# Optimization experiments

Hardware: AMD Instinct MI355X
Metric: run time of the kernel (lower is better)

The kernel has to match this reference:

```python
import jax, jax.numpy as jnp
import numpy as np

H = 2048       # hidden_size
F = 1024       # moe_intermediate_size
E = 32         # n_routed_experts
G = 8          # n_group
TOPK_GROUP = 3
TOP_K = 6      # num_experts_per_tok
N_SHARED = 2
SCALE = 1.0    # routed_scaling_factor
B, S = 1, 2048


def setup_inputs() -> dict:
    key = jax.random.key(0)
    ks = jax.random.split(key, 8)
    std = 0.02
    return {
        "hidden_states": jax.random.normal(ks[0], (B, S, H), dtype=jnp.float32),
        "w_gate": jax.random.normal(ks[1], (E, H), dtype=jnp.float32) * std,
        "wg": jax.random.normal(ks[2], (E, H, F), dtype=jnp.float32) * std,  # stacked gate_proj
        "wu": jax.random.normal(ks[3], (E, H, F), dtype=jnp.float32) * std,  # stacked up_proj
        "wd": jax.random.normal(ks[4], (E, F, H), dtype=jnp.float32) * std,  # stacked down_proj
        "sg": jax.random.normal(ks[5], (N_SHARED * F, H), dtype=jnp.float32) * std,  # shared gate_proj
        "su": jax.random.normal(ks[6], (N_SHARED * F, H), dtype=jnp.float32) * std,  # shared up_proj
        "sd": jax.random.normal(ks[7], (H, N_SHARED * F), dtype=jnp.float32) * std,  # shared down_proj
    }


def reference(hidden_states, w_gate, wg, wu, wd, sg, su, sd):
    b, s, h = hidden_states.shape
    x = hidden_states.reshape(-1, h)                    # [T, H]
    T = x.shape[0]

    # ---- MoEGate (softmax scoring, group_limited_greedy top-k) ----
    logits = x.astype(jnp.float32) @ w_gate.T           # [T, E]
    scores = jax.nn.softmax(logits, axis=-1)
    group_scores = scores.reshape(T, G, E // G).max(axis=-1)          # [T, G]
    _, group_idx = jax.lax.top_k(group_scores, TOPK_GROUP)            # [T, topk_group]
    group_mask = jax.nn.one_hot(group_idx, G, dtype=scores.dtype).sum(axis=1)  # [T, G]
    score_mask = jnp.repeat(group_mask, E // G, axis=-1)              # [T, E]
    tmp_scores = jnp.where(score_mask > 0.5, scores, 0.0)
    topk_weight, topk_idx = jax.lax.top_k(tmp_scores, TOP_K)          # [T, K]
    # norm_topk_prob=True, top_k>1
    topk_weight = topk_weight / (topk_weight.sum(axis=-1, keepdims=True) + 1e-20) * SCALE

    # combine weights per (token, expert): scatter topk weights (indices distinct)
    combine_w = jnp.zeros((T, E), dtype=jnp.float32)
    combine_w = combine_w.at[jnp.arange(T)[:, None], topk_idx].add(topk_weight)

    # ---- routed experts: dense grouped GEMMs, weighted combine ----
    g = jnp.einsum('th,ehf->etf', x, wg)                # [E, T, F]
    u = jnp.einsum('th,ehf->etf', x, wu)                # [E, T, F]
    act = jax.nn.silu(g) * u                            # SiLU gated
    act = act * combine_w.T[:, :, None]                 # fold combine weights before down-proj
    y = jnp.einsum('etf,efh->th', act, wd)              # [T, H]

    # ---- shared experts ----
    shared = (jax.nn.silu(x @ sg.T) * (x @ su.T)) @ sd.T

    return (y + shared).reshape(b, s, h)
```

## Files before the change

kernel.cpp:

```cpp
#include <hip/hip_runtime.h>

#define HD   2048
#define FD   1024
#define NEXP 32
#define TOPK 6
#define TT   2048
#define SDIM 2048
#define NPAIR (TT*TOPK)

typedef __bf16 bf16x8 __attribute__((ext_vector_type(8)));
typedef float  f32x4  __attribute__((ext_vector_type(4)));

#define GLOAD_LDS16(g, l) __builtin_amdgcn_global_load_lds( \
    (const __attribute__((address_space(1))) void*)(g),     \
    (__attribute__((address_space(3))) void*)(l), 16, 0, 0)

#define WAIT_VM3  asm volatile("s_waitcnt vmcnt(3)" ::: "memory")
#define WAIT_VM0  asm volatile("s_waitcnt vmcnt(0)" ::: "memory")
#define BAR() do { __builtin_amdgcn_s_barrier(); } while (0)

__device__ __forceinline__ ushort f2b(float f) {
  __bf16 h = (__bf16)f;
  union { __bf16 h; ushort u; } v; v.h = h;
  return v.u;
}
__device__ __forceinline__ float b2f(ushort u) {
  union { unsigned u; float f; } v; v.u = (unsigned)u << 16;
  return v.f;
}

__device__ __forceinline__ int xcd_swz(int bid, int nact) {
  int xcd = bid & 7, i = bid >> 3;
  int q = nact >> 3, r = nact & 7;
  int base = (xcd < r) ? xcd * (q + 1) : r * (q + 1) + (xcd - r) * q;
  return base + i;
}

__device__ __forceinline__ void argmax32(float &v, int &i) {
  #pragma unroll
  for (int m = 16; m >= 1; m >>= 1) {
    float ov = __shfl_xor(v, m, 32);
    int   oi = __shfl_xor(i, m, 32);
    if (ov > v || (ov == v && oi < i)) { v = ov; i = oi; }
  }
}

__global__ __launch_bounds__(64) void gating_kernel(
    const float* __restrict__ x, const float* __restrict__ wgate,
    int* __restrict__ topk_idx, float* __restrict__ topk_w, int* __restrict__ cnt)
{
  int t = blockIdx.x;
  int l = threadIdx.x;
  int e = l & 31;
  int half = l >> 5;
  const float* xr = x + (size_t)t * HD + half * (HD/2);
  const float* wr = wgate + (size_t)e * HD + half * (HD/2);
  float acc = 0.f;
  for (int i = 0; i < HD/2; i += 4) {
    float4 a = *(const float4*)(xr + i);
    float4 b = *(const float4*)(wr + i);
    acc += a.x*b.x + a.y*b.y + a.z*b.z + a.w*b.w;
  }
  acc += __shfl_xor(acc, 32);
  float logit = acc;
  float mx = logit;
  #pragma unroll
  for (int m = 16; m >= 1; m >>= 1) mx = fmaxf(mx, __shfl_xor(mx, m, 32));
  float p = __expf(logit - mx);
  float s = p;
  #pragma unroll
  for (int m = 16; m >= 1; m >>= 1) s += __shfl_xor(s, m, 32);
  float score = p / s;
  float gs = score;
  gs = fmaxf(gs, __shfl_xor(gs, 1, 32));
  gs = fmaxf(gs, __shfl_xor(gs, 2, 32));
  int g = e >> 2;
  float gw = gs;
  bool ingroup = false;
  for (int r = 0; r < 3; ++r) {
    float v = gw; int gi = g;
    argmax32(v, gi);
    if (g == gi) { ingroup = true; gw = -1.f; }
  }
  float ms = ingroup ? score : 0.f;
  int myrank = -1;
  float denom = 1e-20f;
  float mw = ms;
  for (int r = 0; r < 6; ++r) {
    float v = mw; int ei = e;
    argmax32(v, ei);
    denom += v;
    if (e == ei) { myrank = r; mw = -1.f; }
  }
  if (l < 32 && myrank >= 0) {
    topk_idx[t*TOPK + myrank] = e;
    topk_w  [t*TOPK + myrank] = score / denom;
    atomicAdd(&cnt[e], 1);
  }
}

__global__ void scan_kernel(const int* __restrict__ cnt, int* __restrict__ offs,
                            int* __restrict__ tl_e, int* __restrict__ tl_m, int* __restrict__ ntl) {
  if (threadIdx.x == 0) {
    int o = 0, nt = 0;
    for (int e = 0; e < NEXP; ++e) {
      offs[e] = o;
      for (int m = 0; m < cnt[e]; m += 256) { tl_e[nt] = e; tl_m[nt] = m; ++nt; }
      o += cnt[e];
    }
    ntl[0] = nt;
  }
}

__global__ void fill_kernel(const int* __restrict__ topk_idx, const float* __restrict__ topk_w,
                            const int* __restrict__ offs, int* __restrict__ cur,
                            int* __restrict__ pair_tok, float* __restrict__ pair_w,
                            int* __restrict__ inv)
{
  int idx = blockIdx.x * blockDim.x + threadIdx.x;
  if (idx >= NPAIR) return;
  int e = topk_idx[idx];
  int p = offs[e] + atomicAdd(&cur[e], 1);
  pair_tok[p] = idx / TOPK;
  pair_w[p]   = topk_w[idx];
  inv[idx]    = p;
}

__global__ __launch_bounds__(256) void fconv4(
    const float* __restrict__ s0, const float* __restrict__ s1,
    const float* __restrict__ s2, const float* __restrict__ s3,
    ushort* __restrict__ d0, ushort* __restrict__ d1,
    ushort* __restrict__ d2, ushort* __restrict__ d3)
{
  int sel = blockIdx.y;
  const float* in = (sel == 0) ? s0 : (sel == 1) ? s1 : (sel == 2) ? s2 : s3;
  ushort* out = (sel == 0) ? d0 : (sel == 1) ? d1 : (sel == 2) ? d2 : d3;
  int i = blockIdx.x * blockDim.x + threadIdx.x;
  float4 v = ((const float4*)in)[i];
  ((ushort4*)out)[i] = make_ushort4(f2b(v.x), f2b(v.y), f2b(v.z), f2b(v.w));
}

#define TSTR 76
__global__ __launch_bounds__(256) void tconv2(
    const float* __restrict__ in0, const float* __restrict__ in1,
    ushort* __restrict__ out0, ushort* __restrict__ out1, int R, int C)
{
  __shared__ ushort T[64*TSTR];
  const float* inz = blockIdx.z ? in1 : in0;
  ushort* outz = blockIdx.z ? out1 : out0;
  int tiles_c = C >> 6;
  int bt = blockIdx.x;
  int r0 = (bt / tiles_c) << 6;
  int c0 = (bt % tiles_c) << 6;
  const float* src = inz + (size_t)blockIdx.y * R * C;
  ushort* dst = outz + (size_t)blockIdx.y * R * C;
  int t = threadIdx.x;
  int row = (t >> 4) << 2;
  int col4 = (t & 15) << 2;
  float vv[4][4];
  #pragma unroll
  for (int i = 0; i < 4; ++i) {
    float4 v = *(const float4*)(src + (size_t)(r0 + row + i) * C + c0 + col4);
    vv[i][0] = v.x; vv[i][1] = v.y; vv[i][2] = v.z; vv[i][3] = v.w;
  }
  #pragma unroll
  for (int cc = 0; cc < 4; ++cc)
    *(ushort4*)&T[(col4 + cc)*TSTR + row] =
      make_ushort4(f2b(vv[0][cc]), f2b(vv[1][cc]), f2b(vv[2][cc]), f2b(vv[3][cc]));
  __syncthreads();
  #pragma unroll
  for (int p = 0; p < 2; ++p) {
    int item = t + p*256;
    int oc = item >> 3, seg = item & 7;
    ushort4 a = *(const ushort4*)&T[oc*TSTR + seg*8];
    ushort4 b = *(const ushort4*)&T[oc*TSTR + seg*8 + 4];
    ushort* d = dst + (size_t)(c0 + oc) * R + r0 + seg*8;
    *(ushort4*)(d)     = a;
    *(ushort4*)(d + 4) = b;
  }
}

__global__ __launch_bounds__(256) void combine_kernel(
    const ushort* __restrict__ pairout, const int* __restrict__ inv, float* __restrict__ y)
{
  int t = blockIdx.x;
  int h0 = threadIdx.x * 8;
  const int* iv = inv + t*TOPK;
  float* yr = y + (size_t)t * HD + h0;
  float4 y0 = *(const float4*)(yr);
  float4 y1 = *(const float4*)(yr + 4);
  float acc[8] = {y0.x, y0.y, y0.z, y0.w, y1.x, y1.y, y1.z, y1.w};
  #pragma unroll
  for (int r = 0; r < TOPK; ++r) {
    int p = iv[r];
    const ushort* pr = pairout + (size_t)p * HD + h0;
    ushort4 a = *(const ushort4*)(pr);
    ushort4 b = *(const ushort4*)(pr + 4);
    acc[0] += b2f(a.x); acc[1] += b2f(a.y); acc[2] += b2f(a.z); acc[3] += b2f(a.w);
    acc[4] += b2f(b.x); acc[5] += b2f(b.y); acc[6] += b2f(b.z); acc[7] += b2f(b.w);
  }
  *(float4*)(yr)     = make_float4(acc[0], acc[1], acc[2], acc[3]);
  *(float4*)(yr + 4) = make_float4(acc[4], acc[5], acc[6], acc[7]);
}


__global__ __launch_bounds__(512, 4) void gu_routed_b(
    const ushort* __restrict__ xb, const ushort* __restrict__ wgt, const ushort* __restrict__ wut,
    const int* __restrict__ pair_tok, const float* __restrict__ pair_w,
    const int* __restrict__ cnt, const int* __restrict__ offs,
    const int* __restrict__ tl_e, const int* __restrict__ tl_m, const int* __restrict__ ntl,
    ushort* __restrict__ act)
{
  __shared__ ushort A[3][256*32];
  __shared__ ushort Bg[3][64*32];
  __shared__ ushort Bu[3][64*32];

  int nact = ntl[0] * 16;
  int bid = blockIdx.x;
  if (bid >= nact) return;
  int wid = xcd_swz(bid, nact);
  int tile = wid >> 4;
  int nt = wid & 15;
  int e  = tl_e[tile];
  int m0 = tl_m[tile];
  int ce = cnt[e];
  int oe = offs[e];
  int n0 = nt * 64;
  int tid = threadIdx.x, lane = tid & 63, w = tid >> 6;

  int csrc = (lane & 3) ^ ((lane >> 3) & 3);
  const ushort* asrc[2];
  #pragma unroll
  for (int j = 0; j < 2; ++j) {
    int r = (2*w + j)*16 + (lane >> 2);
    int pi = min(m0 + r, ce - 1);
    asrc[j] = xb + (size_t)pair_tok[oe + pi] * HD + csrc * 8;
  }
  int tsel = w >> 2;
  int bw = w & 3;
  const ushort* bsrc = (tsel ? wut : wgt) +
      ((size_t)e * FD + n0 + bw*16 + (lane >> 2)) * HD + csrc * 8;
  ushort* bdst0 = tsel ? &Bu[0][bw*512] : &Bg[0][bw*512];
  ushort* bdst1 = tsel ? &Bu[1][bw*512] : &Bg[1][bw*512];
  ushort* bdst2 = tsel ? &Bu[2][bw*512] : &Bg[2][bw*512];

  int lm = lane & 15, lg = lane >> 4;
  int wr = w >> 1, wc = w & 1;
  int asw = (lm >> 1) & 3;

  f32x4 accg[4][2], accu[4][2];
  #pragma unroll
  for (int m = 0; m < 4; ++m)
    #pragma unroll
    for (int n = 0; n < 2; ++n) { accg[m][n] = f32x4{0,0,0,0}; accu[m][n] = f32x4{0,0,0,0}; }

  #define GUB_ISSUE(T, BUF, BD) do { \
    GLOAD_LDS16(asrc[0] + (T)*32, &A[BUF][(2*w)*512]); \
    GLOAD_LDS16(asrc[1] + (T)*32, &A[BUF][(2*w+1)*512]); \
    GLOAD_LDS16(bsrc + (T)*32, BD); \
  } while (0)
  #define GUB_COMPUTE(BUF) do { \
    bf16x8 a[4], bg[2], bu[2]; \
    _Pragma("unroll") \
    for (int m = 0; m < 4; ++m) \
      a[m] = *(const bf16x8*)&A[BUF][(wr*64 + m*16 + lm)*32 + (lg ^ asw)*8]; \
    _Pragma("unroll") \
    for (int n = 0; n < 2; ++n) { \
      int row = wc*32 + n*16 + lm; \
      bg[n] = *(const bf16x8*)&Bg[BUF][row*32 + (lg ^ asw)*8]; \
      bu[n] = *(const bf16x8*)&Bu[BUF][row*32 + (lg ^ asw)*8]; \
    } \
    __builtin_amdgcn_s_setprio(1); \
    _Pragma("unroll") \
    for (int m = 0; m < 4; ++m) \
      _Pragma("unroll") \
      for (int n = 0; n < 2; ++n) { \
        accg[m][n] = __builtin_amdgcn_mfma_f32_16x16x32_bf16(a[m], bg[n], accg[m][n], 0, 0, 0); \
        accu[m][n] = __builtin_amdgcn_mfma_f32_16x16x32_bf16(a[m], bu[n], accu[m][n], 0, 0, 0); \
      } \
    __builtin_amdgcn_s_setprio(0); \
  } while (0)

  GUB_ISSUE(0, 0, bdst0);
  GUB_ISSUE(1, 1, bdst1);
  WAIT_VM3;
  BAR();

  for (int tt = 0; tt < 20; ++tt) {
    int t = tt * 3;
    GUB_ISSUE(t+2, 2, bdst2); GUB_COMPUTE(0); WAIT_VM3; BAR();
    GUB_ISSUE(t+3, 0, bdst0); GUB_COMPUTE(1); WAIT_VM3; BAR();
    GUB_ISSUE(t+4, 1, bdst1); GUB_COMPUTE(2); WAIT_VM3; BAR();
  }
  GUB_ISSUE(62, 2, bdst2); GUB_COMPUTE(0); WAIT_VM3; BAR();
  GUB_ISSUE(63, 0, bdst0); GUB_COMPUTE(1); WAIT_VM3; BAR();
  GUB_COMPUTE(2); WAIT_VM0; BAR();
  GUB_COMPUTE(0);
  #undef GUB_ISSUE
  #undef GUB_COMPUTE

  #pragma unroll
  for (int m = 0; m < 4; ++m) {
    #pragma unroll
    for (int j = 0; j < 4; ++j) {
      int rl = wr*64 + m*16 + lg*4 + j;
      int pi = m0 + rl;
      if (pi >= ce) continue;
      float pwv = pair_w[oe + pi];
      size_t base = (size_t)(oe + pi) * FD + n0 + wc*32;
      #pragma unroll
      for (int n = 0; n < 2; ++n) {
        float gv = accg[m][n][j];
        float uv = accu[m][n][j];
        float sv = gv / (1.f + __expf(-gv));
        act[base + n*16 + lm] = f2b(sv * uv * pwv);
      }
    }
  }
}

__global__ __launch_bounds__(512, 4) void down_routed_b(
    const ushort* __restrict__ act, const ushort* __restrict__ wdt,
    const int* __restrict__ cnt, const int* __restrict__ offs,
    const int* __restrict__ tl_e, const int* __restrict__ tl_m, const int* __restrict__ ntl,
    ushort* __restrict__ pairout)
{
  __shared__ ushort A[3][256*32];
  __shared__ ushort Bd[3][128*32];

  int nact = ntl[0] * 16;
  int bid = blockIdx.x;
  if (bid >= nact) return;
  int wid = xcd_swz(bid, nact);
  int tile = wid >> 4;
  int nt = wid & 15;
  int e  = tl_e[tile];
  int m0 = tl_m[tile];
  int ce = cnt[e];
  int oe = offs[e];
  int n0 = nt * 128;
  int tid = threadIdx.x, lane = tid & 63, w = tid >> 6;

  int csrc = (lane & 3) ^ ((lane >> 3) & 3);
  const ushort* asrc[2];
  #pragma unroll
  for (int j = 0; j < 2; ++j) {
    int r = (2*w + j)*16 + (lane >> 2);
    int pi = min(m0 + r, ce - 1);
    asrc[j] = act + (size_t)(oe + pi) * FD + csrc * 8;
  }
  const ushort* bsrc = wdt + ((size_t)e * HD + n0 + w*16 + (lane >> 2)) * FD + csrc * 8;

  int lm = lane & 15, lg = lane >> 4;
  int wr = w >> 1, wc = w & 1;
  int asw = (lm >> 1) & 3;

  f32x4 acc[4][4];
  #pragma unroll
  for (int m = 0; m < 4; ++m)
    #pragma unroll
    for (int n = 0; n < 4; ++n) acc[m][n] = f32x4{0,0,0,0};

  #define DNB_ISSUE(T, BUF) do { \
    GLOAD_LDS16(asrc[0] + (T)*32, &A[BUF][(2*w)*512]); \
    GLOAD_LDS16(asrc[1] + (T)*32, &A[BUF][(2*w+1)*512]); \
    GLOAD_LDS16(bsrc + (T)*32, &Bd[BUF][w*512]); \
  } while (0)
  #define DNB_COMPUTE(BUF) do { \
    bf16x8 a[4], b[4]; \
    _Pragma("unroll") \
    for (int m = 0; m < 4; ++m) \
      a[m] = *(const bf16x8*)&A[BUF][(wr*64 + m*16 + lm)*32 + (lg ^ asw)*8]; \
    _Pragma("unroll") \
    for (int n = 0; n < 4; ++n) { \
      int row = wc*64 + n*16 + lm; \
      b[n] = *(const bf16x8*)&Bd[BUF][row*32 + (lg ^ asw)*8]; \
    } \
    __builtin_amdgcn_s_setprio(1); \
    _Pragma("unroll") \
    for (int m = 0; m < 4; ++m) \
      _Pragma("unroll") \
      for (int n = 0; n < 4; ++n) \
        acc[m][n] = __builtin_amdgcn_mfma_f32_16x16x32_bf16(a[m], b[n], acc[m][n], 0, 0, 0); \
    __builtin_amdgcn_s_setprio(0); \
  } while (0)

  DNB_ISSUE(0, 0);
  DNB_ISSUE(1, 1);
  WAIT_VM3;
  BAR();

  for (int tt = 0; tt < 10; ++tt) {
    int t = tt * 3;
    DNB_ISSUE(t+2, 2); DNB_COMPUTE(0); WAIT_VM3; BAR();
    DNB_ISSUE(t+3, 0); DNB_COMPUTE(1); WAIT_VM3; BAR();
    DNB_ISSUE(t+4, 1); DNB_COMPUTE(2); WAIT_VM3; BAR();
  }
  DNB_COMPUTE(0); WAIT_VM0; BAR();
  DNB_COMPUTE(1);
  #undef DNB_ISSUE
  #undef DNB_COMPUTE

  #pragma unroll
  for (int m = 0; m < 4; ++m) {
    #pragma unroll
    for (int j = 0; j < 4; ++j) {
      int rl = wr*64 + m*16 + lg*4 + j;
      int pi = m0 + rl;
      if (pi >= ce) continue;
      size_t base = (size_t)(oe + pi) * HD + n0 + wc*64;
      #pragma unroll
      for (int n = 0; n < 4; ++n)
        pairout[base + n*16 + lm] = f2b(acc[m][n][j]);
    }
  }
}

__global__ __launch_bounds__(512, 4) void shared_gu_b(
    const ushort* __restrict__ xb, const ushort* __restrict__ sgb, const ushort* __restrict__ sub,
    ushort* __restrict__ sact)
{
  __shared__ ushort A[3][256*32];
  __shared__ ushort Bg[3][64*32];
  __shared__ ushort Bu[3][64*32];

  int bid = blockIdx.x;
  int wid = (bid & 7) * 32 + (bid >> 3);
  int mt = wid & 7;
  int nt = wid >> 3;
  int m0 = mt * 256;
  int n0 = nt * 64;
  int tid = threadIdx.x, lane = tid & 63, w = tid >> 6;

  int csrc = (lane & 3) ^ ((lane >> 3) & 3);
  const ushort* asrc[2];
  #pragma unroll
  for (int j = 0; j < 2; ++j) {
    int r = (2*w + j)*16 + (lane >> 2);
    asrc[j] = xb + (size_t)(m0 + r) * HD + csrc * 8;
  }
  int tsel = w >> 2;
  int bw = w & 3;
  const ushort* bsrc = (tsel ? sub : sgb) + (size_t)(n0 + bw*16 + (lane >> 2)) * HD + csrc * 8;
  ushort* bdst0 = tsel ? &Bu[0][bw*512] : &Bg[0][bw*512];
  ushort* bdst1 = tsel ? &Bu[1][bw*512] : &Bg[1][bw*512];
  ushort* bdst2 = tsel ? &Bu[2][bw*512] : &Bg[2][bw*512];

  int lm = lane & 15, lg = lane >> 4;
  int wr = w >> 1, wc = w & 1;
  int asw = (lm >> 1) & 3;

  f32x4 accg[4][2], accu[4][2];
  #pragma unroll
  for (int m = 0; m < 4; ++m)
    #pragma unroll
    for (int n = 0; n < 2; ++n) { accg[m][n] = f32x4{0,0,0,0}; accu[m][n] = f32x4{0,0,0,0}; }

  #define SGB_ISSUE(T, BUF, BD) do { \
    GLOAD_LDS16(asrc[0] + (T)*32, &A[BUF][(2*w)*512]); \
    GLOAD_LDS16(asrc[1] + (T)*32, &A[BUF][(2*w+1)*512]); \
    GLOAD_LDS16(bsrc + (T)*32, BD); \
  } while (0)
  #define SGB_COMPUTE(BUF) do { \
    bf16x8 a[4], bg[2], bu[2]; \
    _Pragma("unroll") \
    for (int m = 0; m < 4; ++m) \
      a[m] = *(const bf16x8*)&A[BUF][(wr*64 + m*16 + lm)*32 + (lg ^ asw)*8]; \
    _Pragma("unroll") \
    for (int n = 0; n < 2; ++n) { \
      int row = wc*32 + n*16 + lm; \
      bg[n] = *(const bf16x8*)&Bg[BUF][row*32 + (lg ^ asw)*8]; \
      bu[n] = *(const bf16x8*)&Bu[BUF][row*32 + (lg ^ asw)*8]; \
    } \
    __builtin_amdgcn_s_setprio(1); \
    _Pragma("unroll") \
    for (int m = 0; m < 4; ++m) \
      _Pragma("unroll") \
      for (int n = 0; n < 2; ++n) { \
        accg[m][n] = __builtin_amdgcn_mfma_f32_16x16x32_bf16(a[m], bg[n], accg[m][n], 0, 0, 0); \
        accu[m][n] = __builtin_amdgcn_mfma_f32_16x16x32_bf16(a[m], bu[n], accu[m][n], 0, 0, 0); \
      } \
    __builtin_amdgcn_s_setprio(0); \
  } while (0)

  SGB_ISSUE(0, 0, bdst0);
  SGB_ISSUE(1, 1, bdst1);
  WAIT_VM3;
  BAR();

  for (int tt = 0; tt < 20; ++tt) {
    int t = tt * 3;
    SGB_ISSUE(t+2, 2, bdst2); SGB_COMPUTE(0); WAIT_VM3; BAR();
    SGB_ISSUE(t+3, 0, bdst0); SGB_COMPUTE(1); WAIT_VM3; BAR();
    SGB_ISSUE(t+4, 1, bdst1); SGB_COMPUTE(2); WAIT_VM3; BAR();
  }
  SGB_ISSUE(62, 2, bdst2); SGB_COMPUTE(0); WAIT_VM3; BAR();
  SGB_ISSUE(63, 0, bdst0); SGB_COMPUTE(1); WAIT_VM3; BAR();
  SGB_COMPUTE(2); WAIT_VM0; BAR();
  SGB_COMPUTE(0);
  #undef SGB_ISSUE
  #undef SGB_COMPUTE

  #pragma unroll
  for (int m = 0; m < 4; ++m) {
    #pragma unroll
    for (int j = 0; j < 4; ++j) {
      int rl = wr*64 + m*16 + lg*4 + j;
      size_t base = (size_t)(m0 + rl) * SDIM + n0 + wc*32;
      #pragma unroll
      for (int n = 0; n < 2; ++n) {
        float gv = accg[m][n][j];
        float uv = accu[m][n][j];
        float sv = gv / (1.f + __expf(-gv));
        sact[base + n*16 + lm] = f2b(sv * uv);
      }
    }
  }
}

__global__ __launch_bounds__(512, 4) void shared_down_b(
    const ushort* __restrict__ sact, const ushort* __restrict__ sdb, float* __restrict__ y)
{
  __shared__ ushort A[3][256*32];
  __shared__ ushort Bd[3][128*32];

  int bid = blockIdx.x;
  int wid = (bid & 7) * 16 + (bid >> 3);
  int mt = wid & 7;
  int nt = wid >> 3;
  int m0 = mt * 256;
  int n0 = nt * 128;
  int tid = threadIdx.x, lane = tid & 63, w = tid >> 6;

  int csrc = (lane & 3) ^ ((lane >> 3) & 3);
  const ushort* asrc[2];
  #pragma unroll
  for (int j = 0; j < 2; ++j) {
    int r = (2*w + j)*16 + (lane >> 2);
    asrc[j] = sact + (size_t)(m0 + r) * SDIM + csrc * 8;
  }
  const ushort* bsrc = sdb + (size_t)(n0 + w*16 + (lane >> 2)) * SDIM + csrc * 8;

  int lm = lane & 15, lg = lane >> 4;
  int wr = w >> 1, wc = w & 1;
  int asw = (lm >> 1) & 3;

  f32x4 acc[4][4];
  #pragma unroll
  for (int m = 0; m < 4; ++m)
    #pragma unroll
    for (int n = 0; n < 4; ++n) acc[m][n] = f32x4{0,0,0,0};

  #define SDB_ISSUE(T, BUF) do { \
    GLOAD_LDS16(asrc[0] + (T)*32, &A[BUF][(2*w)*512]); \
    GLOAD_LDS16(asrc[1] + (T)*32, &A[BUF][(2*w+1)*512]); \
    GLOAD_LDS16(bsrc + (T)*32, &Bd[BUF][w*512]); \
  } while (0)
  #define SDB_COMPUTE(BUF) do { \
    bf16x8 a[4], b[4]; \
    _Pragma("unroll") \
    for (int m = 0; m < 4; ++m) \
      a[m] = *(const bf16x8*)&A[BUF][(wr*64 + m*16 + lm)*32 + (lg ^ asw)*8]; \
    _Pragma("unroll") \
    for (int n = 0; n < 4; ++n) { \
      int row = wc*64 + n*16 + lm; \
      b[n] = *(const bf16x8*)&Bd[BUF][row*32 + (lg ^ asw)*8]; \
    } \
    __builtin_amdgcn_s_setprio(1); \
    _Pragma("unroll") \
    for (int m = 0; m < 4; ++m) \
      _Pragma("unroll") \
      for (int n = 0; n < 4; ++n) \
        acc[m][n] = __builtin_amdgcn_mfma_f32_16x16x32_bf16(a[m], b[n], acc[m][n], 0, 0, 0); \
    __builtin_amdgcn_s_setprio(0); \
  } while (0)

  SDB_ISSUE(0, 0);
  SDB_ISSUE(1, 1);
  WAIT_VM3;
  BAR();

  for (int tt = 0; tt < 20; ++tt) {
    int t = tt * 3;
    SDB_ISSUE(t+2, 2); SDB_COMPUTE(0); WAIT_VM3; BAR();
    SDB_ISSUE(t+3, 0); SDB_COMPUTE(1); WAIT_VM3; BAR();
    SDB_ISSUE(t+4, 1); SDB_COMPUTE(2); WAIT_VM3; BAR();
  }
  SDB_ISSUE(62, 2); SDB_COMPUTE(0); WAIT_VM3; BAR();
  SDB_ISSUE(63, 0); SDB_COMPUTE(1); WAIT_VM3; BAR();
  SDB_COMPUTE(2); WAIT_VM0; BAR();
  SDB_COMPUTE(0);
  #undef SDB_ISSUE
  #undef SDB_COMPUTE

  #pragma unroll
  for (int m = 0; m < 4; ++m) {
    #pragma unroll
    for (int j = 0; j < 4; ++j) {
      int rl = wr*64 + m*16 + lg*4 + j;
      size_t base = (size_t)(m0 + rl) * HD + n0 + wc*64;
      #pragma unroll
      for (int n = 0; n < 4; ++n)
        y[base + n*16 + lm] = acc[m][n][j];
    }
  }
}

extern "C" void kernel_launch(void* const* d_in, const int* in_sizes, int n_in,
                              void* d_out, int out_size, void* d_ws, size_t ws_size,
                              hipStream_t stream) {
  const float* x     = (const float*)d_in[0];
  const float* wgate = (const float*)d_in[1];
  const float* wg    = (const float*)d_in[2];
  const float* wu    = (const float*)d_in[3];
  const float* wd    = (const float*)d_in[4];
  const float* sg    = (const float*)d_in[5];
  const float* su    = (const float*)d_in[6];
  const float* sd    = (const float*)d_in[7];
  float* y = (float*)d_out;
  char* ws = (char*)d_ws;

  ushort* xb   = (ushort*)(ws + 0);
  ushort* act  = (ushort*)(ws + 8388608);
  ushort* sact = (ushort*)(ws + 33554432);
  int*    tidx = (int*)  (ws + 41943040);
  float*  tw   = (float*)(ws + 41992192);
  int*    ptok = (int*)  (ws + 42041344);
  float*  pw   = (float*)(ws + 42090496);
  int*    cnt  = (int*)  (ws + 42139648);
  int*    curc = (int*)  (ws + 42139776);
  int*    offs = (int*)  (ws + 42139904);
  int*    tl_e = (int*)  (ws + 42140160);
  int*    tl_m = (int*)  (ws + 42140672);
  int*    ntl  = (int*)  (ws + 42141184);
  int*    inv  = (int*)  (ws + 42141440);
  ushort* wgt  = (ushort*)(ws + 50331648);
  ushort* wut  = (ushort*)(ws + 184549376);
  ushort* wdt  = (ushort*)(ws + 318767104);
  ushort* sgb  = (ushort*)(ws + 452984832);
  ushort* sub  = (ushort*)(ws + 461373440);
  ushort* sdb  = (ushort*)(ws + 469762048);
  ushort* pairout = wgt;

  hipMemsetAsync(cnt, 0, 512, stream);

  gating_kernel<<<dim3(TT), dim3(64), 0, stream>>>(x, wgate, tidx, tw, cnt);
  scan_kernel<<<dim3(1), dim3(64), 0, stream>>>(cnt, offs, tl_e, tl_m, ntl);
  fill_kernel<<<dim3(48), dim3(256), 0, stream>>>(tidx, tw, offs, curc, ptok, pw, inv);

  fconv4<<<dim3(4096, 4), dim3(256), 0, stream>>>(x, sg, su, sd, xb, sgb, sub, sdb);
  tconv2<<<dim3(512, NEXP, 2), dim3(256), 0, stream>>>(wg, wu, wgt, wut, HD, FD);
  tconv2<<<dim3(512, NEXP, 1), dim3(256), 0, stream>>>(wd, wd, wdt, wdt, FD, HD);

  shared_gu_b<<<dim3(256), dim3(512), 0, stream>>>(xb, sgb, sub, sact);
  shared_down_b<<<dim3(128), dim3(512), 0, stream>>>(sact, sdb, y);
  gu_routed_b<<<dim3(1280), dim3(512), 0, stream>>>(xb, wgt, wut, ptok, pw, cnt, offs,
                                                    tl_e, tl_m, ntl, act);
  down_routed_b<<<dim3(1280), dim3(512), 0, stream>>>(act, wdt, cnt, offs,
                                                      tl_e, tl_m, ntl, pairout);
  combine_kernel<<<dim3(TT), dim3(256), 0, stream>>>(pairout, inv, y);
}
```

Measured before the change: 733.4 us.

## Load GEMM A operands directly into registers, bypassing LDS, and merge weight transposes

In all four GEMM kernels, the A-operand tile (activations) is no longer staged through LDS. Each wave now loads its own A fragments straight from global memory into registers, double-buffered one K-step ahead, while B still goes through the triple-buffered global-to-LDS path. This cuts LDS footprint and LDS read traffic, but each wave pair now loads the same A rows redundantly and the loads are less coalesced per lane. Separately, the two weight-transpose launches are merged into one three-slice launch to save a kernel launch.

```diff
diff --git a/kernel.cpp b/kernel.cpp
--- a/kernel.cpp
+++ b/kernel.cpp
@@ -15,7 +15,8 @@
     (const __attribute__((address_space(1))) void*)(g),     \
     (__attribute__((address_space(3))) void*)(l), 16, 0, 0)
 
-#define WAIT_VM3  asm volatile("s_waitcnt vmcnt(3)" ::: "memory")
+#define WAIT_VM5  asm volatile("s_waitcnt vmcnt(5)" ::: "memory")
+#define WAIT_VM4  asm volatile("s_waitcnt vmcnt(4)" ::: "memory")
 #define WAIT_VM0  asm volatile("s_waitcnt vmcnt(0)" ::: "memory")
 #define BAR() do { __builtin_amdgcn_s_barrier(); } while (0)
 
@@ -141,13 +142,16 @@
 }
 
 #define TSTR 76
-__global__ __launch_bounds__(256) void tconv2(
-    const float* __restrict__ in0, const float* __restrict__ in1,
-    ushort* __restrict__ out0, ushort* __restrict__ out1, int R, int C)
+__global__ __launch_bounds__(256) void tconv3(
+    const float* __restrict__ iwg, const float* __restrict__ iwu, const float* __restrict__ iwd,
+    ushort* __restrict__ owg, ushort* __restrict__ owu, ushort* __restrict__ owd)
 {
   __shared__ ushort T[64*TSTR];
-  const float* inz = blockIdx.z ? in1 : in0;
-  ushort* outz = blockIdx.z ? out1 : out0;
+  int z = blockIdx.z;
+  const float* inz = (z == 0) ? iwg : (z == 1) ? iwu : iwd;
+  ushort* outz = (z == 0) ? owg : (z == 1) ? owu : owd;
+  int R = (z == 2) ? FD : HD;
+  int C = (z == 2) ? HD : FD;
   int tiles_c = C >> 6;
   int bt = blockIdx.x;
   int r0 = (bt / tiles_c) << 6;
@@ -211,7 +215,6 @@
     const int* __restrict__ tl_e, const int* __restrict__ tl_m, const int* __restrict__ ntl,
     ushort* __restrict__ act)
 {
-  __shared__ ushort A[3][256*32];
   __shared__ ushort Bg[3][64*32];
   __shared__ ushort Bu[3][64*32];
 
@@ -228,14 +231,19 @@
   int n0 = nt * 64;
   int tid = threadIdx.x, lane = tid & 63, w = tid >> 6;
 
+  int lm = lane & 15, lg = lane >> 4;
+  int wr = w >> 1, wc = w & 1;
+  int asw = (lm >> 1) & 3;
+
+  const ushort* ap0; const ushort* ap1; const ushort* ap2; const ushort* ap3;
+  {
+    int r0 = wr*64 + lm;
+    ap0 = xb + (size_t)pair_tok[oe + min(m0 + r0,      ce - 1)] * HD + lg*8;
+    ap1 = xb + (size_t)pair_tok[oe + min(m0 + r0 + 16, ce - 1)] * HD + lg*8;
+    ap2 = xb + (size_t)pair_tok[oe + min(m0 + r0 + 32, ce - 1)] * HD + lg*8;
+    ap3 = xb + (size_t)pair_tok[oe + min(m0 + r0 + 48, ce - 1)] * HD + lg*8;
+  }
   int csrc = (lane & 3) ^ ((lane >> 3) & 3);
-  const ushort* asrc[2];
-  #pragma unroll
-  for (int j = 0; j < 2; ++j) {
-    int r = (2*w + j)*16 + (lane >> 2);
-    int pi = min(m0 + r, ce - 1);
-    asrc[j] = xb + (size_t)pair_tok[oe + pi] * HD + csrc * 8;
-  }
   int tsel = w >> 2;
   int bw = w & 3;
   const ushort* bsrc = (tsel ? wut : wgt) +
@@ -244,26 +252,22 @@
   ushort* bdst1 = tsel ? &Bu[1][bw*512] : &Bg[1][bw*512];
   ushort* bdst2 = tsel ? &Bu[2][bw*512] : &Bg[2][bw*512];
 
-  int lm = lane & 15, lg = lane >> 4;
-  int wr = w >> 1, wc = w & 1;
-  int asw = (lm >> 1) & 3;
-
+  bf16x8 aE0, aE1, aE2, aE3, aO0, aO1, aO2, aO3;
   f32x4 accg[4][2], accu[4][2];
   #pragma unroll
   for (int m = 0; m < 4; ++m)
     #pragma unroll
     for (int n = 0; n < 2; ++n) { accg[m][n] = f32x4{0,0,0,0}; accu[m][n] = f32x4{0,0,0,0}; }
 
-  #define GUB_ISSUE(T, BUF, BD) do { \
-    GLOAD_LDS16(asrc[0] + (T)*32, &A[BUF][(2*w)*512]); \
-    GLOAD_LDS16(asrc[1] + (T)*32, &A[BUF][(2*w+1)*512]); \
-    GLOAD_LDS16(bsrc + (T)*32, BD); \
-  } while (0)
-  #define GUB_COMPUTE(BUF) do { \
-    bf16x8 a[4], bg[2], bu[2]; \
-    _Pragma("unroll") \
-    for (int m = 0; m < 4; ++m) \
-      a[m] = *(const bf16x8*)&A[BUF][(wr*64 + m*16 + lm)*32 + (lg ^ asw)*8]; \
+  #define GUB_ISSUE_B(T, BD) GLOAD_LDS16(bsrc + (T)*32, BD)
+  #define GUB_LOADA(T, A0, A1, A2, A3) do { \
+    A0 = *(const bf16x8*)(ap0 + (T)*32); \
+    A1 = *(const bf16x8*)(ap1 + (T)*32); \
+    A2 = *(const bf16x8*)(ap2 + (T)*32); \
+    A3 = *(const bf16x8*)(ap3 + (T)*32); \
+  } while (0)
+  #define GUB_COMPUTE(BUF, A0, A1, A2, A3) do { \
+    bf16x8 bg[2], bu[2]; \
     _Pragma("unroll") \
     for (int n = 0; n < 2; ++n) { \
       int row = wc*32 + n*16 + lm; \
@@ -272,31 +276,40 @@
     } \
     __builtin_amdgcn_s_setprio(1); \
     _Pragma("unroll") \
-    for (int m = 0; m < 4; ++m) \
-      _Pragma("unroll") \
-      for (int n = 0; n < 2; ++n) { \
-        accg[m][n] = __builtin_amdgcn_mfma_f32_16x16x32_bf16(a[m], bg[n], accg[m][n], 0, 0, 0); \
-        accu[m][n] = __builtin_amdgcn_mfma_f32_16x16x32_bf16(a[m], bu[n], accu[m][n], 0, 0, 0); \
-      } \
+    for (int n = 0; n < 2; ++n) { \
+      accg[0][n] = __builtin_amdgcn_mfma_f32_16x16x32_bf16(A0, bg[n], accg[0][n], 0, 0, 0); \
+      accu[0][n] = __builtin_amdgcn_mfma_f32_16x16x32_bf16(A0, bu[n], accu[0][n], 0, 0, 0); \
+      accg[1][n] = __builtin_amdgcn_mfma_f32_16x16x32_bf16(A1, bg[n], accg[1][n], 0, 0, 0); \
+      accu[1][n] = __builtin_amdgcn_mfma_f32_16x16x32_bf16(A1, bu[n], accu[1][n], 0, 0, 0); \
+      accg[2][n] = __builtin_amdgcn_mfma_f32_16x16x32_bf16(A2, bg[n], accg[2][n], 0, 0, 0); \
+      accu[2][n] = __builtin_amdgcn_mfma_f32_16x16x32_bf16(A2, bu[n], accu[2][n], 0, 0, 0); \
+      accg[3][n] = __builtin_amdgcn_mfma_f32_16x16x32_bf16(A3, bg[n], accg[3][n], 0, 0, 0); \
+      accu[3][n] = __builtin_amdgcn_mfma_f32_16x16x32_bf16(A3, bu[n], accu[3][n], 0, 0, 0); \
+    } \
     __builtin_amdgcn_s_setprio(0); \
   } while (0)
 
-  GUB_ISSUE(0, 0, bdst0);
-  GUB_ISSUE(1, 1, bdst1);
-  WAIT_VM3;
+  GUB_ISSUE_B(0, bdst0);
+  GUB_ISSUE_B(1, bdst1);
+  GUB_LOADA(0, aE0, aE1, aE2, aE3);
+  WAIT_VM5;
   BAR();
 
-  for (int tt = 0; tt < 20; ++tt) {
-    int t = tt * 3;
-    GUB_ISSUE(t+2, 2, bdst2); GUB_COMPUTE(0); WAIT_VM3; BAR();
-    GUB_ISSUE(t+3, 0, bdst0); GUB_COMPUTE(1); WAIT_VM3; BAR();
-    GUB_ISSUE(t+4, 1, bdst1); GUB_COMPUTE(2); WAIT_VM3; BAR();
-  }
-  GUB_ISSUE(62, 2, bdst2); GUB_COMPUTE(0); WAIT_VM3; BAR();
-  GUB_ISSUE(63, 0, bdst0); GUB_COMPUTE(1); WAIT_VM3; BAR();
-  GUB_COMPUTE(2); WAIT_VM0; BAR();
-  GUB_COMPUTE(0);
-  #undef GUB_ISSUE
+  for (int tt = 0; tt < 10; ++tt) {
+    int t = tt * 6;
+    GUB_ISSUE_B(t+2, bdst2); GUB_LOADA(t+1, aO0,aO1,aO2,aO3); GUB_COMPUTE(0, aE0,aE1,aE2,aE3); WAIT_VM5; BAR();
+    GUB_ISSUE_B(t+3, bdst0); GUB_LOADA(t+2, aE0,aE1,aE2,aE3); GUB_COMPUTE(1, aO0,aO1,aO2,aO3); WAIT_VM5; BAR();
+    GUB_ISSUE_B(t+4, bdst1); GUB_LOADA(t+3, aO0,aO1,aO2,aO3); GUB_COMPUTE(2, aE0,aE1,aE2,aE3); WAIT_VM5; BAR();
+    GUB_ISSUE_B(t+5, bdst2); GUB_LOADA(t+4, aE0,aE1,aE2,aE3); GUB_COMPUTE(0, aO0,aO1,aO2,aO3); WAIT_VM5; BAR();
+    GUB_ISSUE_B(t+6, bdst0); GUB_LOADA(t+5, aO0,aO1,aO2,aO3); GUB_COMPUTE(1, aE0,aE1,aE2,aE3); WAIT_VM5; BAR();
+    GUB_ISSUE_B(t+7, bdst1); GUB_LOADA(t+6, aE0,aE1,aE2,aE3); GUB_COMPUTE(2, aO0,aO1,aO2,aO3); WAIT_VM5; BAR();
+  }
+  GUB_ISSUE_B(62, bdst2); GUB_LOADA(61, aO0,aO1,aO2,aO3); GUB_COMPUTE(0, aE0,aE1,aE2,aE3); WAIT_VM5; BAR();
+  GUB_ISSUE_B(63, bdst0); GUB_LOADA(62, aE0,aE1,aE2,aE3); GUB_COMPUTE(1, aO0,aO1,aO2,aO3); WAIT_VM5; BAR();
+  GUB_LOADA(63, aO0,aO1,aO2,aO3); GUB_COMPUTE(2, aE0,aE1,aE2,aE3); WAIT_VM4; BAR();
+  GUB_COMPUTE(0, aO0,aO1,aO2,aO3);
+  #undef GUB_ISSUE_B
+  #undef GUB_LOADA
   #undef GUB_COMPUTE
 
   #pragma unroll
@@ -325,7 +338,6 @@
     const int* __restrict__ tl_e, const int* __restrict__ tl_m, const int* __restrict__ ntl,
     ushort* __restrict__ pairout)
 {
-  __shared__ ushort A[3][256*32];
   __shared__ ushort Bd[3][128*32];
 
   int nact = ntl[0] * 16;
@@ -341,36 +353,37 @@
   int n0 = nt * 128;
   int tid = threadIdx.x, lane = tid & 63, w = tid >> 6;
 
-  int csrc = (lane & 3) ^ ((lane >> 3) & 3);
-  const ushort* asrc[2];
-  #pragma unroll
-  for (int j = 0; j < 2; ++j) {
-    int r = (2*w + j)*16 + (lane >> 2);
-    int pi = min(m0 + r, ce - 1);
-    asrc[j] = act + (size_t)(oe + pi) * FD + csrc * 8;
-  }
-  const ushort* bsrc = wdt + ((size_t)e * HD + n0 + w*16 + (lane >> 2)) * FD + csrc * 8;
-
   int lm = lane & 15, lg = lane >> 4;
   int wr = w >> 1, wc = w & 1;
   int asw = (lm >> 1) & 3;
 
+  const ushort* ap0; const ushort* ap1; const ushort* ap2; const ushort* ap3;
+  {
+    int r0 = wr*64 + lm;
+    ap0 = act + (size_t)(oe + min(m0 + r0,      ce - 1)) * FD + lg*8;
+    ap1 = act + (size_t)(oe + min(m0 + r0 + 16, ce - 1)) * FD + lg*8;
+    ap2 = act + (size_t)(oe + min(m0 + r0 + 32, ce - 1)) * FD + lg*8;
+    ap3 = act + (size_t)(oe + min(m0 + r0 + 48, ce - 1)) * FD + lg*8;
+  }
+  int csrc = (lane & 3) ^ ((lane >> 3) & 3);
+  const ushort* bsrc = wdt + ((size_t)e * HD + n0 + w*16 + (lane >> 2)) * FD + csrc * 8;
+
+  bf16x8 aE0, aE1, aE2, aE3, aO0, aO1, aO2, aO3;
   f32x4 acc[4][4];
   #pragma unroll
   for (int m = 0; m < 4; ++m)
     #pragma unroll
     for (int n = 0; n < 4; ++n) acc[m][n] = f32x4{0,0,0,0};
 
-  #define DNB_ISSUE(T, BUF) do { \
-    GLOAD_LDS16(asrc[0] + (T)*32, &A[BUF][(2*w)*512]); \
-    GLOAD_LDS16(asrc[1] + (T)*32, &A[BUF][(2*w+1)*512]); \
-    GLOAD_LDS16(bsrc + (T)*32, &Bd[BUF][w*512]); \
-  } while (0)
-  #define DNB_COMPUTE(BUF) do { \
-    bf16x8 a[4], b[4]; \
-    _Pragma("unroll") \
-    for (int m = 0; m < 4; ++m) \
-      a[m] = *(const bf16x8*)&A[BUF][(wr*64 + m*16 + lm)*32 + (lg ^ asw)*8]; \
+  #define DNB_ISSUE_B(T, BUF) GLOAD_LDS16(bsrc + (T)*32, &Bd[BUF][w*512])
+  #define DNB_LOADA(T, A0, A1, A2, A3) do { \
+    A0 = *(const bf16x8*)(ap0 + (T)*32); \
+    A1 = *(const bf16x8*)(ap1 + (T)*32); \
+    A2 = *(const bf16x8*)(ap2 + (T)*32); \
+    A3 = *(const bf16x8*)(ap3 + (T)*32); \
+  } while (0)
+  #define DNB_COMPUTE(BUF, A0, A1, A2, A3) do { \
+    bf16x8 b[4]; \
     _Pragma("unroll") \
     for (int n = 0; n < 4; ++n) { \
       int row = wc*64 + n*16 + lm; \
@@ -378,27 +391,34 @@
     } \
     __builtin_amdgcn_s_setprio(1); \
     _Pragma("unroll") \
-    for (int m = 0; m < 4; ++m) \
-      _Pragma("unroll") \
-      for (int n = 0; n < 4; ++n) \
-        acc[m][n] = __builtin_amdgcn_mfma_f32_16x16x32_bf16(a[m], b[n], acc[m][n], 0, 0, 0); \
+    for (int n = 0; n < 4; ++n) { \
+      acc[0][n] = __builtin_amdgcn_mfma_f32_16x16x32_bf16(A0, b[n], acc[0][n], 0, 0, 0); \
+      acc[1][n] = __builtin_amdgcn_mfma_f32_16x16x32_bf16(A1, b[n], acc[1][n], 0, 0, 0); \
+      acc[2][n] = __builtin_amdgcn_mfma_f32_16x16x32_bf16(A2, b[n], acc[2][n], 0, 0, 0); \
+      acc[3][n] = __builtin_amdgcn_mfma_f32_16x16x32_bf16(A3, b[n], acc[3][n], 0, 0, 0); \
+    } \
     __builtin_amdgcn_s_setprio(0); \
   } while (0)
 
-  DNB_ISSUE(0, 0);
-  DNB_ISSUE(1, 1);
-  WAIT_VM3;
+  DNB_ISSUE_B(0, 0);
+  DNB_ISSUE_B(1, 1);
+  DNB_LOADA(0, aE0, aE1, aE2, aE3);
+  WAIT_VM5;
   BAR();
 
-  for (int tt = 0; tt < 10; ++tt) {
-    int t = tt * 3;
-    DNB_ISSUE(t+2, 2); DNB_COMPUTE(0); WAIT_VM3; BAR();
-    DNB_ISSUE(t+3, 0); DNB_COMPUTE(1); WAIT_VM3; BAR();
-    DNB_ISSUE(t+4, 1); DNB_COMPUTE(2); WAIT_VM3; BAR();
-  }
-  DNB_COMPUTE(0); WAIT_VM0; BAR();
-  DNB_COMPUTE(1);
-  #undef DNB_ISSUE
+  for (int tt = 0; tt < 5; ++tt) {
+    int t = tt * 6;
+    DNB_ISSUE_B(t+2, 2); DNB_LOADA(t+1, aO0,aO1,aO2,aO3); DNB_COMPUTE(0, aE0,aE1,aE2,aE3); WAIT_VM5; BAR();
+    DNB_ISSUE_B(t+3, 0); DNB_LOADA(t+2, aE0,aE1,aE2,aE3); DNB_COMPUTE(1, aO0,aO1,aO2,aO3); WAIT_VM5; BAR();
+    DNB_ISSUE_B(t+4, 1); DNB_LOADA(t+3, aO0,aO1,aO2,aO3); DNB_COMPUTE(2, aE0,aE1,aE2,aE3); WAIT_VM5; BAR();
+    DNB_ISSUE_B(t+5, 2); DNB_LOADA(t+4, aE0,aE1,aE2,aE3); DNB_COMPUTE(0, aO0,aO1,aO2,aO3); WAIT_VM5; BAR();
+    DNB_ISSUE_B(t+6, 0); DNB_LOADA(t+5, aO0,aO1,aO2,aO3); DNB_COMPUTE(1, aE0,aE1,aE2,aE3); WAIT_VM5; BAR();
+    DNB_ISSUE_B(t+7, 1); DNB_LOADA(t+6, aE0,aE1,aE2,aE3); DNB_COMPUTE(2, aO0,aO1,aO2,aO3); WAIT_VM5; BAR();
+  }
+  DNB_LOADA(31, aO0,aO1,aO2,aO3); DNB_COMPUTE(0, aE0,aE1,aE2,aE3); WAIT_VM4; BAR();
+  DNB_COMPUTE(1, aO0,aO1,aO2,aO3);
+  #undef DNB_ISSUE_B
+  #undef DNB_LOADA
   #undef DNB_COMPUTE
 
   #pragma unroll
@@ -420,7 +440,6 @@
     const ushort* __restrict__ xb, const ushort* __restrict__ sgb, const ushort* __restrict__ sub,
     ushort* __restrict__ sact)
 {
-  __shared__ ushort A[3][256*32];
   __shared__ ushort Bg[3][64*32];
   __shared__ ushort Bu[3][64*32];
 
@@ -432,13 +451,19 @@
   int n0 = nt * 64;
   int tid = threadIdx.x, lane = tid & 63, w = tid >> 6;
 
+  int lm = lane & 15, lg = lane >> 4;
+  int wr = w >> 1, wc = w & 1;
+  int asw = (lm >> 1) & 3;
+
+  const ushort* ap0; const ushort* ap1; const ushort* ap2; const ushort* ap3;
+  {
+    int r0 = m0 + wr*64 + lm;
+    ap0 = xb + (size_t)(r0)      * HD + lg*8;
+    ap1 = xb + (size_t)(r0 + 16) * HD + lg*8;
+    ap2 = xb + (size_t)(r0 + 32) * HD + lg*8;
+    ap3 = xb + (size_t)(r0 + 48) * HD + lg*8;
+  }
   int csrc = (lane & 3) ^ ((lane >> 3) & 3);
-  const ushort* asrc[2];
-  #pragma unroll
-  for (int j = 0; j < 2; ++j) {
-    int r = (2*w + j)*16 + (lane >> 2);
-    asrc[j] = xb + (size_t)(m0 + r) * HD + csrc * 8;
-  }
   int tsel = w >> 2;
   int bw = w & 3;
   const ushort* bsrc = (tsel ? sub : sgb) + (size_t)(n0 + bw*16 + (lane >> 2)) * HD + csrc * 8;
@@ -446,26 +471,22 @@
   ushort* bdst1 = tsel ? &Bu[1][bw*512] : &Bg[1][bw*512];
   ushort* bdst2 = tsel ? &Bu[2][bw*512] : &Bg[2][bw*512];
 
-  int lm = lane & 15, lg = lane >> 4;
-  int wr = w >> 1, wc = w & 1;
-  int asw = (lm >> 1) & 3;
-
+  bf16x8 aE0, aE1, aE2, aE3, aO0, aO1, aO2, aO3;
   f32x4 accg[4][2], accu[4][2];
   #pragma unroll
   for (int m = 0; m < 4; ++m)
     #pragma unroll
     for (int n = 0; n < 2; ++n) { accg[m][n] = f32x4{0,0,0,0}; accu[m][n] = f32x4{0,0,0,0}; }
 
-  #define SGB_ISSUE(T, BUF, BD) do { \
-    GLOAD_LDS16(asrc[0] + (T)*32, &A[BUF][(2*w)*512]); \
-    GLOAD_LDS16(asrc[1] + (T)*32, &A[BUF][(2*w+1)*512]); \
-    GLOAD_LDS16(bsrc + (T)*32, BD); \
-  } while (0)
-  #define SGB_COMPUTE(BUF) do { \
-    bf16x8 a[4], bg[2], bu[2]; \
-    _Pragma("unroll") \
-    for (int m = 0; m < 4; ++m) \
-      a[m] = *(const bf16x8*)&A[BUF][(wr*64 + m*16 + lm)*32 + (lg ^ asw)*8]; \
+  #define SGB_ISSUE_B(T, BD) GLOAD_LDS16(bsrc + (T)*32, BD)
+  #define SGB_LOADA(T, A0, A1, A2, A3) do { \
+    A0 = *(const bf16x8*)(ap0 + (T)*32); \
+    A1 = *(const bf16x8*)(ap1 + (T)*32); \
+    A2 = *(const bf16x8*)(ap2 + (T)*32); \
+    A3 = *(const bf16x8*)(ap3 + (T)*32); \
+  } while (0)
+  #define SGB_COMPUTE(BUF, A0, A1, A2, A3) do { \
+    bf16x8 bg[2], bu[2]; \
     _Pragma("unroll") \
     for (int n = 0; n < 2; ++n) { \
       int row = wc*32 + n*16 + lm; \
@@ -474,31 +495,40 @@
     } \
     __builtin_amdgcn_s_setprio(1); \
     _Pragma("unroll") \
-    for (int m = 0; m < 4; ++m) \
-      _Pragma("unroll") \
-      for (int n = 0; n < 2; ++n) { \
-        accg[m][n] = __builtin_amdgcn_mfma_f32_16x16x32_bf16(a[m], bg[n], accg[m][n], 0, 0, 0); \
-        accu[m][n] = __builtin_amdgcn_mfma_f32_16x16x32_bf16(a[m], bu[n], accu[m][n], 0, 0, 0); \
-      } \
+    for (int n = 0; n < 2; ++n) { \
+      accg[0][n] = __builtin_amdgcn_mfma_f32_16x16x32_bf16(A0, bg[n], accg[0][n], 0, 0, 0); \
+      accu[0][n] = __builtin_amdgcn_mfma_f32_16x16x32_bf16(A0, bu[n], accu[0][n], 0, 0, 0); \
+      accg[1][n] = __builtin_amdgcn_mfma_f32_16x16x32_bf16(A1, bg[n], accg[1][n], 0, 0, 0); \
+      accu[1][n] = __builtin_amdgcn_mfma_f32_16x16x32_bf16(A1, bu[n], accu[1][n], 0, 0, 0); \
+      accg[2][n] = __builtin_amdgcn_mfma_f32_16x16x32_bf16(A2, bg[n], accg[2][n], 0, 0, 0); \
+      accu[2][n] = __builtin_amdgcn_mfma_f32_16x16x32_bf16(A2, bu[n], accu[2][n], 0, 0, 0); \
+      accg[3][n] = __builtin_amdgcn_mfma_f32_16x16x32_bf16(A3, bg[n], accg[3][n], 0, 0, 0); \
+      accu[3][n] = __builtin_amdgcn_mfma_f32_16x16x32_bf16(A3, bu[n], accu[3][n], 0, 0, 0); \
+    } \
     __builtin_amdgcn_s_setprio(0); \
   } while (0)
 
-  SGB_ISSUE(0, 0, bdst0);
-  SGB_ISSUE(1, 1, bdst1);
-  WAIT_VM3;
+  SGB_ISSUE_B(0, bdst0);
+  SGB_ISSUE_B(1, bdst1);
+  SGB_LOADA(0, aE0, aE1, aE2, aE3);
+  WAIT_VM5;
   BAR();
 
-  for (int tt = 0; tt < 20; ++tt) {
-    int t = tt * 3;
-    SGB_ISSUE(t+2, 2, bdst2); SGB_COMPUTE(0); WAIT_VM3; BAR();
-    SGB_ISSUE(t+3, 0, bdst0); SGB_COMPUTE(1); WAIT_VM3; BAR();
-    SGB_ISSUE(t+4, 1, bdst1); SGB_COMPUTE(2); WAIT_VM3; BAR();
-  }
-  SGB_ISSUE(62, 2, bdst2); SGB_COMPUTE(0); WAIT_VM3; BAR();
-  SGB_ISSUE(63, 0, bdst0); SGB_COMPUTE(1); WAIT_VM3; BAR();
-  SGB_COMPUTE(2); WAIT_VM0; BAR();
-  SGB_COMPUTE(0);
-  #undef SGB_ISSUE
+  for (int tt = 0; tt < 10; ++tt) {
+    int t = tt * 6;
+    SGB_ISSUE_B(t+2, bdst2); SGB_LOADA(t+1, aO0,aO1,aO2,aO3); SGB_COMPUTE(0, aE0,aE1,aE2,aE3); WAIT_VM5; BAR();
+    SGB_ISSUE_B(t+3, bdst0); SGB_LOADA(t+2, aE0,aE1,aE2,aE3); SGB_COMPUTE(1, aO0,aO1,aO2,aO3); WAIT_VM5; BAR();
+    SGB_ISSUE_B(t+4, bdst1); SGB_LOADA(t+3, aO0,aO1,aO2,aO3); SGB_COMPUTE(2, aE0,aE1,aE2,aE3); WAIT_VM5; BAR();
+    SGB_ISSUE_B(t+5, bdst2); SGB_LOADA(t+4, aE0,aE1,aE2,aE3); SGB_COMPUTE(0, aO0,aO1,aO2,aO3); WAIT_VM5; BAR();
+    SGB_ISSUE_B(t+6, bdst0); SGB_LOADA(t+5, aO0,aO1,aO2,aO3); SGB_COMPUTE(1, aE0,aE1,aE2,aE3); WAIT_VM5; BAR();
+    SGB_ISSUE_B(t+7, bdst1); SGB_LOADA(t+6, aE0,aE1,aE2,aE3); SGB_COMPUTE(2, aO0,aO1,aO2,aO3); WAIT_VM5; BAR();
+  }
+  SGB_ISSUE_B(62, bdst2); SGB_LOADA(61, aO0,aO1,aO2,aO3); SGB_COMPUTE(0, aE0,aE1,aE2,aE3); WAIT_VM5; BAR();
+  SGB_ISSUE_B(63, bdst0); SGB_LOADA(62, aE0,aE1,aE2,aE3); SGB_COMPUTE(1, aO0,aO1,aO2,aO3); WAIT_VM5; BAR();
+  SGB_LOADA(63, aO0,aO1,aO2,aO3); SGB_COMPUTE(2, aE0,aE1,aE2,aE3); WAIT_VM4; BAR();
+  SGB_COMPUTE(0, aO0,aO1,aO2,aO3);
+  #undef SGB_ISSUE_B
+  #undef SGB_LOADA
   #undef SGB_COMPUTE
 
   #pragma unroll
@@ -521,7 +551,6 @@
 __global__ __launch_bounds__(512, 4) void shared_down_b(
     const ushort* __restrict__ sact, const ushort* __restrict__ sdb, float* __restrict__ y)
 {
-  __shared__ ushort A[3][256*32];
   __shared__ ushort Bd[3][128*32];
 
   int bid = blockIdx.x;
@@ -532,35 +561,37 @@
   int n0 = nt * 128;
   int tid = threadIdx.x, lane = tid & 63, w = tid >> 6;
 
-  int csrc = (lane & 3) ^ ((lane >> 3) & 3);
-  const ushort* asrc[2];
-  #pragma unroll
-  for (int j = 0; j < 2; ++j) {
-    int r = (2*w + j)*16 + (lane >> 2);
-    asrc[j] = sact + (size_t)(m0 + r) * SDIM + csrc * 8;
-  }
-  const ushort* bsrc = sdb + (size_t)(n0 + w*16 + (lane >> 2)) * SDIM + csrc * 8;
-
   int lm = lane & 15, lg = lane >> 4;
   int wr = w >> 1, wc = w & 1;
   int asw = (lm >> 1) & 3;
 
+  const ushort* ap0; const ushort* ap1; const ushort* ap2; const ushort* ap3;
+  {
+    int r0 = m0 + wr*64 + lm;
+    ap0 = sact + (size_t)(r0)      * SDIM + lg*8;
+    ap1 = sact + (size_t)(r0 + 16) * SDIM + lg*8;
+    ap2 = sact + (size_t)(r0 + 32) * SDIM + lg*8;
+    ap3 = sact + (size_t)(r0 + 48) * SDIM + lg*8;
+  }
+  int csrc = (lane & 3) ^ ((lane >> 3) & 3);
+  const ushort* bsrc = sdb + (size_t)(n0 + w*16 + (lane >> 2)) * SDIM + csrc * 8;
+
+  bf16x8 aE0, aE1, aE2, aE3, aO0, aO1, aO2, aO3;
   f32x4 acc[4][4];
   #pragma unroll
   for (int m = 0; m < 4; ++m)
     #pragma unroll
     for (int n = 0; n < 4; ++n) acc[m][n] = f32x4{0,0,0,0};
 
-  #define SDB_ISSUE(T, BUF) do { \
-    GLOAD_LDS16(asrc[0] + (T)*32, &A[BUF][(2*w)*512]); \
-    GLOAD_LDS16(asrc[1] + (T)*32, &A[BUF][(2*w+1)*512]); \
-    GLOAD_LDS16(bsrc + (T)*32, &Bd[BUF][w*512]); \
-  } while (0)
-  #define SDB_COMPUTE(BUF) do { \
-    bf16x8 a[4], b[4]; \
-    _Pragma("unroll") \
-    for (int m = 0; m < 4; ++m) \
-      a[m] = *(const bf16x8*)&A[BUF][(wr*64 + m*16 + lm)*32 + (lg ^ asw)*8]; \
+  #define SDB_ISSUE_B(T, BUF) GLOAD_LDS16(bsrc + (T)*32, &Bd[BUF][w*512])
+  #define SDB_LOADA(T, A0, A1, A2, A3) do { \
+    A0 = *(const bf16x8*)(ap0 + (T)*32); \
+    A1 = *(const bf16x8*)(ap1 + (T)*32); \
+    A2 = *(const bf16x8*)(ap2 + (T)*32); \
+    A3 = *(const bf16x8*)(ap3 + (T)*32); \
+  } while (0)
+  #define SDB_COMPUTE(BUF, A0, A1, A2, A3) do { \
+    bf16x8 b[4]; \
     _Pragma("unroll") \
     for (int n = 0; n < 4; ++n) { \
       int row = wc*64 + n*16 + lm; \
@@ -568,29 +599,36 @@
     } \
     __builtin_amdgcn_s_setprio(1); \
     _Pragma("unroll") \
-    for (int m = 0; m < 4; ++m) \
-      _Pragma("unroll") \
-      for (int n = 0; n < 4; ++n) \
-        acc[m][n] = __builtin_amdgcn_mfma_f32_16x16x32_bf16(a[m], b[n], acc[m][n], 0, 0, 0); \
+    for (int n = 0; n < 4; ++n) { \
+      acc[0][n] = __builtin_amdgcn_mfma_f32_16x16x32_bf16(A0, b[n], acc[0][n], 0, 0, 0); \
+      acc[1][n] = __builtin_amdgcn_mfma_f32_16x16x32_bf16(A1, b[n], acc[1][n], 0, 0, 0); \
+      acc[2][n] = __builtin_amdgcn_mfma_f32_16x16x32_bf16(A2, b[n], acc[2][n], 0, 0, 0); \
+      acc[3][n] = __builtin_amdgcn_mfma_f32_16x16x32_bf16(A3, b[n], acc[3][n], 0, 0, 0); \
+    } \
     __builtin_amdgcn_s_setprio(0); \
   } while (0)
 
-  SDB_ISSUE(0, 0);
-  SDB_ISSUE(1, 1);
-  WAIT_VM3;
+  SDB_ISSUE_B(0, 0);
+  SDB_ISSUE_B(1, 1);
+  SDB_LOADA(0, aE0, aE1, aE2, aE3);
+  WAIT_VM5;
   BAR();
 
-  for (int tt = 0; tt < 20; ++tt) {
-    int t = tt * 3;
-    SDB_ISSUE(t+2, 2); SDB_COMPUTE(0); WAIT_VM3; BAR();
-    SDB_ISSUE(t+3, 0); SDB_COMPUTE(1); WAIT_VM3; BAR();
-    SDB_ISSUE(t+4, 1); SDB_COMPUTE(2); WAIT_VM3; BAR();
-  }
-  SDB_ISSUE(62, 2); SDB_COMPUTE(0); WAIT_VM3; BAR();
-  SDB_ISSUE(63, 0); SDB_COMPUTE(1); WAIT_VM3; BAR();
-  SDB_COMPUTE(2); WAIT_VM0; BAR();
-  SDB_COMPUTE(0);
-  #undef SDB_ISSUE
+  for (int tt = 0; tt < 10; ++tt) {
+    int t = tt * 6;
+    SDB_ISSUE_B(t+2, 2); SDB_LOADA(t+1, aO0,aO1,aO2,aO3); SDB_COMPUTE(0, aE0,aE1,aE2,aE3); WAIT_VM5; BAR();
+    SDB_ISSUE_B(t+3, 0); SDB_LOADA(t+2, aE0,aE1,aE2,aE3); SDB_COMPUTE(1, aO0,aO1,aO2,aO3); WAIT_VM5; BAR();
+    SDB_ISSUE_B(t+4, 1); SDB_LOADA(t+3, aO0,aO1,aO2,aO3); SDB_COMPUTE(2, aE0,aE1,aE2,aE3); WAIT_VM5; BAR();
+    SDB_ISSUE_B(t+5, 2); SDB_LOADA(t+4, aE0,aE1,aE2,aE3); SDB_COMPUTE(0, aO0,aO1,aO2,aO3); WAIT_VM5; BAR();
+    SDB_ISSUE_B(t+6, 0); SDB_LOADA(t+5, aO0,aO1,aO2,aO3); SDB_COMPUTE(1, aE0,aE1,aE2,aE3); WAIT_VM5; BAR();
+    SDB_ISSUE_B(t+7, 1); SDB_LOADA(t+6, aE0,aE1,aE2,aE3); SDB_COMPUTE(2, aO0,aO1,aO2,aO3); WAIT_VM5; BAR();
+  }
+  SDB_ISSUE_B(62, 2); SDB_LOADA(61, aO0,aO1,aO2,aO3); SDB_COMPUTE(0, aE0,aE1,aE2,aE3); WAIT_VM5; BAR();
+  SDB_ISSUE_B(63, 0); SDB_LOADA(62, aE0,aE1,aE2,aE3); SDB_COMPUTE(1, aO0,aO1,aO2,aO3); WAIT_VM5; BAR();
+  SDB_LOADA(63, aO0,aO1,aO2,aO3); SDB_COMPUTE(2, aE0,aE1,aE2,aE3); WAIT_VM4; BAR();
+  SDB_COMPUTE(0, aO0,aO1,aO2,aO3);
+  #undef SDB_ISSUE_B
+  #undef SDB_LOADA
   #undef SDB_COMPUTE
 
   #pragma unroll
@@ -649,8 +687,7 @@
   fill_kernel<<<dim3(48), dim3(256), 0, stream>>>(tidx, tw, offs, curc, ptok, pw, inv);
 
   fconv4<<<dim3(4096, 4), dim3(256), 0, stream>>>(x, sg, su, sd, xb, sgb, sub, sdb);
-  tconv2<<<dim3(512, NEXP, 2), dim3(256), 0, stream>>>(wg, wu, wgt, wut, HD, FD);
-  tconv2<<<dim3(512, NEXP, 1), dim3(256), 0, stream>>>(wd, wd, wdt, wdt, FD, HD);
+  tconv3<<<dim3(512, NEXP, 3), dim3(256), 0, stream>>>(wg, wu, wd, wgt, wut, wdt);
 
   shared_gu_b<<<dim3(256), dim3(512), 0, stream>>>(xb, sgb, sub, sact);
   shared_down_b<<<dim3(128), dim3(512), 0, stream>>>(sact, sdb, y);
```

Measured after the change: 996.2 us. +35.8%, slower.
